# Optimization experiments

Hardware: AMD Instinct MI355X
Metric: run time of the kernel (lower is better)

The kernel has to match this reference:

```python
import jax, jax.numpy as jnp
import numpy as np

H = 256        # hidden_size
MAX_LEN = 200  # position table has MAX_LEN+1 rows
B = 4096       # number of sessions


def setup_inputs() -> dict:
    rng = np.random.RandomState(0)
    # ragged session lengths in [10, 100)
    seq_len = rng.randint(10, 100, size=B).astype(np.int64)
    T = int(seq_len.sum())
    # reverse positions: len-1, ..., 1, 0 per session (as the torch code uses)
    reverse_pos = np.concatenate([np.arange(l - 1, -1, -1) for l in seq_len]).astype(np.int64)

    key = jax.random.key(0)
    ks = jax.random.split(key, 8)
    def lin(k, fin, fout):
        # torch Linear init ~ U(-1/sqrt(fin), 1/sqrt(fin)); store as [fin, fout]
        lim = 1.0 / np.sqrt(fin)
        kw, kb = jax.random.split(k)
        W = jax.random.uniform(kw, (fin, fout), jnp.float32, -lim, lim)
        b = jax.random.uniform(kb, (fout,), jnp.float32, -lim, lim)
        return W, b

    hidden = jax.random.normal(ks[0], (T, H), jnp.float32)
    pos_table = jax.random.normal(ks[1], (MAX_LEN + 1, H), jnp.float32)
    W_pos, b_pos = lin(ks[2], 2 * H, H)   # W_pos_inter
    W1, b1 = lin(ks[3], H, H)             # W_1_inter
    W2, b2 = lin(ks[4], H, H)             # W_2_inter
    qw, qb = lin(ks[5], H, 1)             # q_inter

    return {
        "hidden": hidden,
        "pos_table": pos_table,
        "W_pos": W_pos, "b_pos": b_pos,
        "W1": W1, "b1": b1,
        "W2": W2, "b2": b2,
        "qw": qw, "qb": qb,
        "seq_len": jnp.asarray(seq_len),
        "reverse_pos": jnp.asarray(reverse_pos),
    }


def reference(hidden, pos_table, W_pos, b_pos, W1, b1, W2, b2, qw, qb, seq_len, reverse_pos):
    T = hidden.shape[0]
    nb = seq_len.shape[0]
    # segment id per token (sessions are contiguous)
    seg = jnp.repeat(jnp.arange(nb), seq_len, total_repeat_length=T)  # [T]
    # per-session mean, gathered back per token (v_mean_repeat_concat)
    sess_mean = jax.ops.segment_sum(hidden, seg, num_segments=nb)
    sess_mean = sess_mean / seq_len[:, None].astype(hidden.dtype)
    v_mean = sess_mean[seg]                                           # [T, H]
    # position-augmented hidden: tanh(W_pos_inter([hidden; pos_emb]))
    pos_emb = pos_table[reverse_pos]                                  # [T, H]
    pos_hidden = jnp.tanh(jnp.concatenate([hidden, pos_emb], -1) @ W_pos + b_pos)
    # alpha = q_inter(sigmoid(W_1_inter(v_mean) + W_2_inter(pos_hidden)))
    gate = jax.nn.sigmoid(v_mean @ W1 + b1 + pos_hidden @ W2 + b2)
    alpha = gate @ qw + qb                                            # [T, 1]
    # per-session weighted sum of hidden
    h_s = jax.ops.segment_sum(alpha * hidden, seg, num_segments=nb)   # [B, H]
    return h_s
```

## Files before the change

### kernel.cpp

```cpp
#include <hip/hip_runtime.h>
#include <hip/hip_bf16.h>
#include <stdint.h>

#define HD 256
#define BM 64
#define APAD 8
#define ASTRIDE (HD + APAD)

typedef __bf16 bf16x8 __attribute__((ext_vector_type(8)));
typedef float f32x4 __attribute__((ext_vector_type(4)));
typedef unsigned short ushort8v __attribute__((ext_vector_type(8)));
typedef unsigned short us4 __attribute__((ext_vector_type(4)));

__device__ __forceinline__ unsigned short f2bf(float f) {
    unsigned int x = __float_as_uint(f);
    unsigned int r = (x + 0x7FFFu + ((x >> 16) & 1u)) >> 16;
    return (unsigned short)r;
}

__global__ void scan_kernel(const int* __restrict__ seq_len, int* __restrict__ offsets, int B) {
    __shared__ int sums[256];
    int tid = threadIdx.x;
    int per = (B + 255) / 256;
    int b0 = tid * per;
    int local[32];
    int tot = 0;
    for (int i = 0; i < per && i < 32; ++i) {
        int b = b0 + i;
        int v = (b < B) ? seq_len[b] : 0;
        local[i] = tot;
        tot += v;
    }
    sums[tid] = tot;
    __syncthreads();
    for (int off = 1; off < 256; off <<= 1) {
        int v = (tid >= off) ? sums[tid - off] : 0;
        __syncthreads();
        sums[tid] += v;
        __syncthreads();
    }
    int start = sums[tid] - tot;
    for (int i = 0; i < per && i < 32; ++i) {
        int b = b0 + i;
        if (b < B) offsets[b] = start + local[i];
    }
    if (tid == 255) offsets[B] = sums[255];
}

__global__ void mean_kernel(const float* __restrict__ hidden, const int* __restrict__ offsets,
                            unsigned short* __restrict__ mean_bf, unsigned short* __restrict__ hb,
                            int* __restrict__ seg) {
    int b = blockIdx.x;
    int s = offsets[b], e = offsets[b + 1];
    int tid = threadIdx.x;
    for (int t = s + tid; t < e; t += 256) seg[t] = b;
    int g = tid >> 6, c = tid & 63;
    float4 acc = {0.f, 0.f, 0.f, 0.f};
    for (int t = s + g; t < e; t += 4) {
        const float4 v = *reinterpret_cast<const float4*>(hidden + (size_t)t * HD + c * 4);
        acc.x += v.x; acc.y += v.y; acc.z += v.z; acc.w += v.w;
        if (hb) {
            us4 pk;
            pk[0] = f2bf(v.x); pk[1] = f2bf(v.y); pk[2] = f2bf(v.z); pk[3] = f2bf(v.w);
            *reinterpret_cast<us4*>(hb + (size_t)t * HD + c * 4) = pk;
        }
    }
    __shared__ float4 part[4][64];
    part[g][c] = acc;
    __syncthreads();
    if (g == 0) {
        float4 a0 = part[0][c], a1 = part[1][c], a2 = part[2][c], a3 = part[3][c];
        float inv = 1.0f / (float)(e - s);
        us4 pk;
        pk[0] = f2bf((a0.x + a1.x + a2.x + a3.x) * inv);
        pk[1] = f2bf((a0.y + a1.y + a2.y + a3.y) * inv);
        pk[2] = f2bf((a0.z + a1.z + a2.z + a3.z) * inv);
        pk[3] = f2bf((a0.w + a1.w + a2.w + a3.w) * inv);
        *reinterpret_cast<us4*>(mean_bf + (size_t)b * HD + c * 4) = pk;
    }
}

__global__ void transpose_kernel(const float* __restrict__ Wp, const float* __restrict__ W1,
                                 const float* __restrict__ W2,
                                 unsigned short* __restrict__ WphT, unsigned short* __restrict__ WpbT,
                                 unsigned short* __restrict__ W1T, unsigned short* __restrict__ W2T) {
    __shared__ unsigned short tile[64][72];
    int bid = blockIdx.x;
    int tid = threadIdx.x;
    const float* src;
    unsigned short* dst;
    int k0, n0, kk;
    if (bid < 32) {
        int tk = bid >> 2, tn = bid & 3;
        src = Wp; k0 = tk * 64; n0 = tn * 64;
        if (k0 < 256) { dst = WphT; kk = k0; }
        else          { dst = WpbT; kk = k0 - 256; }
    } else if (bid < 48) {
        int b2 = bid - 32;
        src = W1; k0 = (b2 >> 2) * 64; n0 = (b2 & 3) * 64;
        dst = W1T; kk = k0;
    } else {
        int b2 = bid - 48;
        src = W2; k0 = (b2 >> 2) * 64; n0 = (b2 & 3) * 64;
        dst = W2T; kk = k0;
    }
    {
        int col = tid & 63;
        int rbase = tid >> 6;
        #pragma unroll
        for (int i = 0; i < 16; ++i) {
            int lrow = rbase + 4 * i;
            tile[lrow][col] = f2bf(src[(size_t)(k0 + lrow) * HD + n0 + col]);
        }
    }
    __syncthreads();
    {
        int nl = tid >> 2;
        int kc0 = (tid & 3) * 16;
        #pragma unroll
        for (int j = 0; j < 4; ++j) {
            int kc = kc0 + 4 * j;
            us4 v;
            v[0] = tile[kc + 0][nl];
            v[1] = tile[kc + 1][nl];
            v[2] = tile[kc + 2][nl];
            v[3] = tile[kc + 3][nl];
            *reinterpret_cast<us4*>(dst + (size_t)(n0 + nl) * HD + kk + kc) = v;
        }
    }
}

__global__ __launch_bounds__(256) void small_gemm_kernel(
    const unsigned short* __restrict__ mean_bf, int Mu, int nbu,
    const float* __restrict__ pos_table, int Mp,
    const unsigned short* __restrict__ W1T, const unsigned short* __restrict__ WpbT,
    const float* __restrict__ b1, const float* __restrict__ b2, const float* __restrict__ bp,
    float* __restrict__ u, float* __restrict__ P2) {
    __shared__ __align__(16) unsigned short As[16][ASTRIDE];
    int tid = threadIdx.x;
    bool isU = (int)blockIdx.x < nbu;
    int m0 = isU ? blockIdx.x * 16 : (blockIdx.x - nbu) * 16;
    int M  = isU ? Mu : Mp;
    const unsigned short* BT = isU ? W1T : WpbT;
    float* out = isU ? u : P2;

    {
        int row = tid >> 4;
        int colg = (tid & 15) * 16;
        int m = m0 + row;
        if (isU) {
            ushort8v v0 = {0,0,0,0,0,0,0,0}, v1 = {0,0,0,0,0,0,0,0};
            if (m < M) {
                v0 = *reinterpret_cast<const ushort8v*>(mean_bf + (size_t)m * HD + colg);
                v1 = *reinterpret_cast<const ushort8v*>(mean_bf + (size_t)m * HD + colg + 8);
            }
            *reinterpret_cast<ushort8v*>(&As[row][colg])     = v0;
            *reinterpret_cast<ushort8v*>(&As[row][colg + 8]) = v1;
        } else {
            float4 f[4] = {{0,0,0,0},{0,0,0,0},{0,0,0,0},{0,0,0,0}};
            if (m < M) {
                const float4* p = reinterpret_cast<const float4*>(pos_table + (size_t)m * HD + colg);
                f[0] = p[0]; f[1] = p[1]; f[2] = p[2]; f[3] = p[3];
            }
            ushort8v v0, v1;
            v0[0]=f2bf(f[0].x); v0[1]=f2bf(f[0].y); v0[2]=f2bf(f[0].z); v0[3]=f2bf(f[0].w);
            v0[4]=f2bf(f[1].x); v0[5]=f2bf(f[1].y); v0[6]=f2bf(f[1].z); v0[7]=f2bf(f[1].w);
            v1[0]=f2bf(f[2].x); v1[1]=f2bf(f[2].y); v1[2]=f2bf(f[2].z); v1[3]=f2bf(f[2].w);
            v1[4]=f2bf(f[3].x); v1[5]=f2bf(f[3].y); v1[6]=f2bf(f[3].z); v1[7]=f2bf(f[3].w);
            *reinterpret_cast<ushort8v*>(&As[row][colg])     = v0;
            *reinterpret_cast<ushort8v*>(&As[row][colg + 8]) = v1;
        }
    }
    __syncthreads();

    int wave = tid >> 6, lane = tid & 63, quad = lane >> 4, cc = lane & 15;
    int nb = wave * 64;
    f32x4 acc4[4];
    for (int i = 0; i < 4; ++i) acc4[i] = (f32x4){0.f, 0.f, 0.f, 0.f};

    bf16x8 wfp[4];
    for (int nf = 0; nf < 4; ++nf)
        wfp[nf] = *reinterpret_cast<const bf16x8*>(BT + (size_t)(nb + nf * 16 + cc) * HD + quad * 8);
    for (int kc8 = 0; kc8 < 8; ++kc8) {
        int kc = kc8 * 32;
        bf16x8 wfc[4];
        for (int nf = 0; nf < 4; ++nf) wfc[nf] = wfp[nf];
        if (kc8 < 7)
            for (int nf = 0; nf < 4; ++nf)
                wfp[nf] = *reinterpret_cast<const bf16x8*>(BT + (size_t)(nb + nf * 16 + cc) * HD + kc + 32 + quad * 8);
        bf16x8 af = *reinterpret_cast<const bf16x8*>(&As[cc][kc + quad * 8]);
        for (int nf = 0; nf < 4; ++nf)
            acc4[nf] = __builtin_amdgcn_mfma_f32_16x16x32_bf16(af, wfc[nf], acc4[nf], 0, 0, 0);
    }
    for (int nf = 0; nf < 4; ++nf)
        for (int r = 0; r < 4; ++r) {
            int row = m0 + quad * 4 + r;
            int col = nb + nf * 16 + cc;
            if (row < M) {
                float bias = isU ? (b1[col] + b2[col]) : bp[col];
                out[(size_t)row * HD + col] = acc4[nf][r] + bias;
            }
        }
}

__global__ __launch_bounds__(512, 4) void main_kernel(
    const float* __restrict__ hidden, const unsigned short* __restrict__ hb, int T,
    const unsigned short* __restrict__ WphT,
    const unsigned short* __restrict__ W2T,
    const float* __restrict__ P2,
    const float* __restrict__ u,
    const float* __restrict__ qw, const float* __restrict__ qb,
    const int* __restrict__ rp, const int* __restrict__ seg,
    float* __restrict__ alpha) {
    __shared__ __align__(16) unsigned short Ah[BM][ASTRIDE];
    __shared__ int rp_s[BM];
    __shared__ int seg_s[BM];
    __shared__ float alpha_s[BM];

    int tid = threadIdx.x;
    int t0 = blockIdx.x * BM;
    int wave = tid >> 6, lane = tid & 63, quad = lane >> 4, cc = lane & 15;
    int mb = wave * 32;

    bf16x8 afp[2];
    #pragma unroll
    for (int mf = 0; mf < 2; ++mf)
        afp[mf] = *reinterpret_cast<const bf16x8*>(WphT + (size_t)(mb + mf * 16 + cc) * HD + quad * 8);

    {
        int row = tid >> 3;
        int t = t0 + row;
        if (hb) {
            #pragma unroll
            for (int i = 0; i < 4; ++i) {
                int cg = (tid & 7) * 8 + 64 * i;
                ushort8v v = {0,0,0,0,0,0,0,0};
                if (t < T) v = *reinterpret_cast<const ushort8v*>(hb + (size_t)t * HD + cg);
                *reinterpret_cast<ushort8v*>(&Ah[row][cg]) = v;
            }
        } else {
            #pragma unroll
            for (int i = 0; i < 4; ++i) {
                int cg = (tid & 7) * 8 + 64 * i;
                float4 f0 = {0,0,0,0}, f1 = {0,0,0,0};
                if (t < T) {
                    const float4* p = reinterpret_cast<const float4*>(hidden + (size_t)t * HD + cg);
                    f0 = p[0]; f1 = p[1];
                }
                ushort8v pk;
                pk[0] = f2bf(f0.x); pk[1] = f2bf(f0.y); pk[2] = f2bf(f0.z); pk[3] = f2bf(f0.w);
                pk[4] = f2bf(f1.x); pk[5] = f2bf(f1.y); pk[6] = f2bf(f1.z); pk[7] = f2bf(f1.w);
                *reinterpret_cast<ushort8v*>(&Ah[row][cg]) = pk;
            }
        }
    }
    if (tid < BM) {
        int t = t0 + tid;
        rp_s[tid]  = (t < T) ? rp[t] : 0;
        seg_s[tid] = (t < T) ? seg[t] : 0;
        alpha_s[tid] = qb[0];
    }
    __syncthreads();

    f32x4 acc[2][4];
    #pragma unroll
    for (int i = 0; i < 2; ++i)
        #pragma unroll
        for (int j = 0; j < 4; ++j) acc[i][j] = (f32x4){0.f, 0.f, 0.f, 0.f};

    for (int kc8 = 0; kc8 < 8; ++kc8) {
        int kc = kc8 * 32;
        bf16x8 afc[2];
        #pragma unroll
        for (int mf = 0; mf < 2; ++mf) afc[mf] = afp[mf];
        if (kc8 < 7)
            #pragma unroll
            for (int mf = 0; mf < 2; ++mf)
                afp[mf] = *reinterpret_cast<const bf16x8*>(WphT + (size_t)(mb + mf * 16 + cc) * HD + kc + 32 + quad * 8);
        bf16x8 bfr[4];
        #pragma unroll
        for (int nf = 0; nf < 4; ++nf)
            bfr[nf] = *reinterpret_cast<const bf16x8*>(&Ah[nf * 16 + cc][kc + quad * 8]);
        #pragma unroll
        for (int mf = 0; mf < 2; ++mf)
            #pragma unroll
            for (int nf = 0; nf < 4; ++nf)
                acc[mf][nf] = __builtin_amdgcn_mfma_f32_16x16x32_bf16(afc[mf], bfr[nf], acc[mf][nf], 0, 0, 0);
    }
    __syncthreads();

    bf16x8 wfp[2];
    #pragma unroll
    for (int mf = 0; mf < 2; ++mf)
        wfp[mf] = *reinterpret_cast<const bf16x8*>(W2T + (size_t)(mb + mf * 16 + cc) * HD + quad * 8);

    #pragma unroll
    for (int nf = 0; nf < 4; ++nf) {
        int token = nf * 16 + cc;
        const float* p2row = P2 + (size_t)rp_s[token] * HD;
        #pragma unroll
        for (int mf = 0; mf < 2; ++mf) {
            int h0 = mb + mf * 16 + quad * 4;
            const float4 p2v = *reinterpret_cast<const float4*>(p2row + h0);
            us4 pk;
            {
                float v0 = acc[mf][nf][0] + p2v.x;
                float v1 = acc[mf][nf][1] + p2v.y;
                float v2 = acc[mf][nf][2] + p2v.z;
                float v3 = acc[mf][nf][3] + p2v.w;
                float e0 = __expf(2.f * v0), e1 = __expf(2.f * v1);
                float e2 = __expf(2.f * v2), e3 = __expf(2.f * v3);
                pk[0] = f2bf(1.f - 2.f / (e0 + 1.f));
                pk[1] = f2bf(1.f - 2.f / (e1 + 1.f));
                pk[2] = f2bf(1.f - 2.f / (e2 + 1.f));
                pk[3] = f2bf(1.f - 2.f / (e3 + 1.f));
            }
            *reinterpret_cast<us4*>(&Ah[token][h0]) = pk;
            acc[mf][nf] = (f32x4){0.f, 0.f, 0.f, 0.f};
        }
    }
    __syncthreads();

    for (int kc8 = 0; kc8 < 8; ++kc8) {
        int kc = kc8 * 32;
        bf16x8 wfc[2];
        #pragma unroll
        for (int mf = 0; mf < 2; ++mf) wfc[mf] = wfp[mf];
        if (kc8 < 7)
            #pragma unroll
            for (int mf = 0; mf < 2; ++mf)
                wfp[mf] = *reinterpret_cast<const bf16x8*>(W2T + (size_t)(mb + mf * 16 + cc) * HD + kc + 32 + quad * 8);
        #pragma unroll
        for (int nf = 0; nf < 4; ++nf) {
            bf16x8 af = *reinterpret_cast<const bf16x8*>(&Ah[nf * 16 + cc][kc + quad * 8]);
            #pragma unroll
            for (int mf = 0; mf < 2; ++mf)
                acc[mf][nf] = __builtin_amdgcn_mfma_f32_16x16x32_bf16(wfc[mf], af, acc[mf][nf], 0, 0, 0);
        }
    }

    float4 qv[2];
    #pragma unroll
    for (int mf = 0; mf < 2; ++mf)
        qv[mf] = *reinterpret_cast<const float4*>(qw + mb + mf * 16 + quad * 4);
    #pragma unroll
    for (int nf = 0; nf < 4; ++nf) {
        int token = nf * 16 + cc;
        const float* urow = u + (size_t)seg_s[token] * HD;
        float s = 0.f;
        #pragma unroll
        for (int mf = 0; mf < 2; ++mf) {
            int n0 = mb + mf * 16 + quad * 4;
            const float4 uv = *reinterpret_cast<const float4*>(urow + n0);
            #pragma unroll
            for (int r = 0; r < 4; ++r) {
                float g = acc[mf][nf][r] + ((const float*)&uv)[r];
                g = 1.0f / (1.0f + __expf(-g));
                s += g * ((const float*)&qv[mf])[r];
            }
        }
        s += __shfl_xor(s, 16);
        s += __shfl_xor(s, 32);
        if (quad == 0) atomicAdd(&alpha_s[token], s);
    }
    __syncthreads();
    if (tid < BM) {
        int t = t0 + tid;
        if (t < T) alpha[t] = alpha_s[tid];
    }
}

__global__ void hs_kernel(const float* __restrict__ hidden, const unsigned short* __restrict__ hb,
                          const float* __restrict__ alpha,
                          const int* __restrict__ offsets, float* __restrict__ out) {
    int b = blockIdx.x;
    int s = offsets[b], e = offsets[b + 1];
    int tid = threadIdx.x;
    __shared__ float al[256];
    for (int i = tid; i < e - s; i += 256) al[i] = alpha[s + i];
    __syncthreads();
    int g = tid >> 6, c = tid & 63;
    float4 acc = {0.f, 0.f, 0.f, 0.f};
    if (hb) {
        for (int t = s + g; t < e; t += 4) {
            float a = al[t - s];
            us4 v = *reinterpret_cast<const us4*>(hb + (size_t)t * HD + c * 4);
            acc.x += a * __uint_as_float(((unsigned)v[0]) << 16);
            acc.y += a * __uint_as_float(((unsigned)v[1]) << 16);
            acc.z += a * __uint_as_float(((unsigned)v[2]) << 16);
            acc.w += a * __uint_as_float(((unsigned)v[3]) << 16);
        }
    } else {
        for (int t = s + g; t < e; t += 4) {
            float a = al[t - s];
            const float4 v = *reinterpret_cast<const float4*>(hidden + (size_t)t * HD + c * 4);
            acc.x += a * v.x; acc.y += a * v.y; acc.z += a * v.z; acc.w += a * v.w;
        }
    }
    __shared__ float4 part[4][64];
    part[g][c] = acc;
    __syncthreads();
    if (g == 0) {
        float4 a0 = part[0][c], a1 = part[1][c], a2 = part[2][c], a3 = part[3][c];
        float4 m;
        m.x = a0.x + a1.x + a2.x + a3.x;
        m.y = a0.y + a1.y + a2.y + a3.y;
        m.z = a0.z + a1.z + a2.z + a3.z;
        m.w = a0.w + a1.w + a2.w + a3.w;
        *reinterpret_cast<float4*>(out + (size_t)b * HD + c * 4) = m;
    }
}

extern "C" void kernel_launch(void* const* d_in, const int* in_sizes, int n_in,
                              void* d_out, int out_size, void* d_ws, size_t ws_size,
                              hipStream_t stream) {
    (void)n_in; (void)out_size;
    const float* hidden    = (const float*)d_in[0];
    const float* pos_table = (const float*)d_in[1];
    const float* W_pos     = (const float*)d_in[2];
    const float* b_pos     = (const float*)d_in[3];
    const float* W1        = (const float*)d_in[4];
    const float* b1        = (const float*)d_in[5];
    const float* W2        = (const float*)d_in[6];
    const float* b2        = (const float*)d_in[7];
    const float* qw        = (const float*)d_in[8];
    const float* qb        = (const float*)d_in[9];
    const int* seq_len     = (const int*)d_in[10];
    const int* reverse_pos = (const int*)d_in[11];

    int T  = in_sizes[0] / HD;
    int B  = in_sizes[10];
    int NP = in_sizes[1] / HD;

    char* ws = (char*)d_ws;
    char* ws_end = ws + ws_size;
    auto carve = [&](size_t bytes) -> char* {
        char* p = ws;
        ws += (bytes + 255) & ~(size_t)255;
        return p;
    };
    int* offsets          = (int*)carve((size_t)(B + 1) * sizeof(int));
    int* seg              = (int*)carve((size_t)T * sizeof(int));
    unsigned short* meanb = (unsigned short*)carve((size_t)B * HD * 2);
    float* u              = (float*)carve((size_t)B * HD * sizeof(float));
    float* P2             = (float*)carve((size_t)NP * HD * sizeof(float));
    unsigned short* WphT  = (unsigned short*)carve((size_t)HD * HD * 2);
    unsigned short* WpbT  = (unsigned short*)carve((size_t)HD * HD * 2);
    unsigned short* W1T   = (unsigned short*)carve((size_t)HD * HD * 2);
    unsigned short* W2T   = (unsigned short*)carve((size_t)HD * HD * 2);
    float* alpha          = (float*)carve((size_t)T * sizeof(float));
    unsigned short* hb    = nullptr;
    if ((size_t)(ws_end - ws) >= (size_t)T * HD * 2 + 256)
        hb = (unsigned short*)carve((size_t)T * HD * 2);

    int nbu = (B + 15) / 16;
    int nbp = (NP + 15) / 16;

    scan_kernel<<<1, 256, 0, stream>>>(seq_len, offsets, B);
    transpose_kernel<<<64, 256, 0, stream>>>(W_pos, W1, W2, WphT, WpbT, W1T, W2T);
    mean_kernel<<<B, 256, 0, stream>>>(hidden, offsets, meanb, hb, seg);
    small_gemm_kernel<<<nbu + nbp, 256, 0, stream>>>(meanb, B, nbu, pos_table, NP,
                                                     W1T, WpbT, b1, b2, b_pos, u, P2);
    main_kernel<<<(T + BM - 1) / BM, 512, 0, stream>>>(hidden, hb, T, WphT, W2T, P2, u, qw, qb,
                                                       reverse_pos, seg, alpha);
    hs_kernel<<<B, 256, 0, stream>>>(hidden, hb, alpha, offsets, (float*)d_out);
}
```

Baseline: 561.1 us.

## Merge prep kernels, use one wave per session, prefetch gathered rows

Merges the scan and weight-transpose kernels into one launch. The mean and weighted-sum kernels now give each session a single wavefront that walks its tokens serially, which removes the shared-memory partial reduction and block barriers. In the main kernel, the gathered P2 and u rows are loaded early so their latency overlaps the MFMA loops. The trade-off is less memory-level parallelism per session in the reduction kernels and higher register pressure in the main kernel.

```diff
diff --git a/kernel.cpp b/kernel.cpp
--- a/kernel.cpp
+++ b/kernel.cpp
@@ -18,116 +18,117 @@
     return (unsigned short)r;
 }
 
-__global__ void scan_kernel(const int* __restrict__ seq_len, int* __restrict__ offsets, int B) {
-    __shared__ int sums[256];
+__global__ void prep_kernel(const int* __restrict__ seq_len, int* __restrict__ offsets, int B,
+                            const float* __restrict__ Wp, const float* __restrict__ W1,
+                            const float* __restrict__ W2,
+                            unsigned short* __restrict__ WphT, unsigned short* __restrict__ WpbT,
+                            unsigned short* __restrict__ W1T, unsigned short* __restrict__ W2T) {
     int tid = threadIdx.x;
-    int per = (B + 255) / 256;
-    int b0 = tid * per;
-    int local[32];
-    int tot = 0;
-    for (int i = 0; i < per && i < 32; ++i) {
-        int b = b0 + i;
-        int v = (b < B) ? seq_len[b] : 0;
-        local[i] = tot;
-        tot += v;
-    }
-    sums[tid] = tot;
-    __syncthreads();
-    for (int off = 1; off < 256; off <<= 1) {
-        int v = (tid >= off) ? sums[tid - off] : 0;
+    if (blockIdx.x == 0) {
+        __shared__ int sums[256];
+        int per = (B + 255) / 256;
+        int b0 = tid * per;
+        int local[32];
+        int tot = 0;
+        for (int i = 0; i < per && i < 32; ++i) {
+            int b = b0 + i;
+            int v = (b < B) ? seq_len[b] : 0;
+            local[i] = tot;
+            tot += v;
+        }
+        sums[tid] = tot;
         __syncthreads();
-        sums[tid] += v;
+        for (int off = 1; off < 256; off <<= 1) {
+            int v = (tid >= off) ? sums[tid - off] : 0;
+            __syncthreads();
+            sums[tid] += v;
+            __syncthreads();
+        }
+        int start = sums[tid] - tot;
+        for (int i = 0; i < per && i < 32; ++i) {
+            int b = b0 + i;
+            if (b < B) offsets[b] = start + local[i];
+        }
+        if (tid == 255) offsets[B] = sums[255];
+    } else {
+        __shared__ unsigned short tile[64][72];
+        int bid = blockIdx.x - 1;
+        const float* src;
+        unsigned short* dst;
+        int k0, n0, kk;
+        if (bid < 32) {
+            int tk = bid >> 2, tn = bid & 3;
+            src = Wp; k0 = tk * 64; n0 = tn * 64;
+            if (k0 < 256) { dst = WphT; kk = k0; }
+            else          { dst = WpbT; kk = k0 - 256; }
+        } else if (bid < 48) {
+            int b2 = bid - 32;
+            src = W1; k0 = (b2 >> 2) * 64; n0 = (b2 & 3) * 64;
+            dst = W1T; kk = k0;
+        } else {
+            int b2 = bid - 48;
+            src = W2; k0 = (b2 >> 2) * 64; n0 = (b2 & 3) * 64;
+            dst = W2T; kk = k0;
+        }
+        {
+            int col = tid & 63;
+            int rbase = tid >> 6;
+            #pragma unroll
+            for (int i = 0; i < 16; ++i) {
+                int lrow = rbase + 4 * i;
+                tile[lrow][col] = f2bf(src[(size_t)(k0 + lrow) * HD + n0 + col]);
+            }
+        }
         __syncthreads();
-    }
-    int start = sums[tid] - tot;
-    for (int i = 0; i < per && i < 32; ++i) {
-        int b = b0 + i;
-        if (b < B) offsets[b] = start + local[i];
-    }
-    if (tid == 255) offsets[B] = sums[255];
-}
-
-__global__ void mean_kernel(const float* __restrict__ hidden, const int* __restrict__ offsets,
-                            unsigned short* __restrict__ mean_bf, unsigned short* __restrict__ hb,
-                            int* __restrict__ seg) {
-    int b = blockIdx.x;
+        {
+            int nl = tid >> 2;
+            int kc0 = (tid & 3) * 16;
+            #pragma unroll
+            for (int j = 0; j < 4; ++j) {
+                int kc = kc0 + 4 * j;
+                us4 v;
+                v[0] = tile[kc + 0][nl];
+                v[1] = tile[kc + 1][nl];
+                v[2] = tile[kc + 2][nl];
+                v[3] = tile[kc + 3][nl];
+                *reinterpret_cast<us4*>(dst + (size_t)(n0 + nl) * HD + kk + kc) = v;
+            }
+        }
+    }
+}
+
+__global__ __launch_bounds__(256) void mean_kernel(
+    const float* __restrict__ hidden, const int* __restrict__ offsets,
+    unsigned short* __restrict__ mean_bf, unsigned short* __restrict__ hb,
+    int* __restrict__ seg, int B) {
+    int wave = threadIdx.x >> 6, lane = threadIdx.x & 63;
+    int b = blockIdx.x * 4 + wave;
+    if (b >= B) return;
     int s = offsets[b], e = offsets[b + 1];
-    int tid = threadIdx.x;
-    for (int t = s + tid; t < e; t += 256) seg[t] = b;
-    int g = tid >> 6, c = tid & 63;
+    for (int t = s + lane; t < e; t += 64) seg[t] = b;
+    int c4 = lane * 4;
     float4 acc = {0.f, 0.f, 0.f, 0.f};
-    for (int t = s + g; t < e; t += 4) {
-        const float4 v = *reinterpret_cast<const float4*>(hidden + (size_t)t * HD + c * 4);
-        acc.x += v.x; acc.y += v.y; acc.z += v.z; acc.w += v.w;
-        if (hb) {
+    if (hb) {
+        for (int t = s; t < e; ++t) {
+            const float4 v = *reinterpret_cast<const float4*>(hidden + (size_t)t * HD + c4);
+            acc.x += v.x; acc.y += v.y; acc.z += v.z; acc.w += v.w;
             us4 pk;
             pk[0] = f2bf(v.x); pk[1] = f2bf(v.y); pk[2] = f2bf(v.z); pk[3] = f2bf(v.w);
-            *reinterpret_cast<us4*>(hb + (size_t)t * HD + c * 4) = pk;
-        }
-    }
-    __shared__ float4 part[4][64];
-    part[g][c] = acc;
-    __syncthreads();
-    if (g == 0) {
-        float4 a0 = part[0][c], a1 = part[1][c], a2 = part[2][c], a3 = part[3][c];
-        float inv = 1.0f / (float)(e - s);
-        us4 pk;
-        pk[0] = f2bf((a0.x + a1.x + a2.x + a3.x) * inv);
-        pk[1] = f2bf((a0.y + a1.y + a2.y + a3.y) * inv);
-        pk[2] = f2bf((a0.z + a1.z + a2.z + a3.z) * inv);
-        pk[3] = f2bf((a0.w + a1.w + a2.w + a3.w) * inv);
-        *reinterpret_cast<us4*>(mean_bf + (size_t)b * HD + c * 4) = pk;
-    }
-}
-
-__global__ void transpose_kernel(const float* __restrict__ Wp, const float* __restrict__ W1,
-                                 const float* __restrict__ W2,
-                                 unsigned short* __restrict__ WphT, unsigned short* __restrict__ WpbT,
-                                 unsigned short* __restrict__ W1T, unsigned short* __restrict__ W2T) {
-    __shared__ unsigned short tile[64][72];
-    int bid = blockIdx.x;
-    int tid = threadIdx.x;
-    const float* src;
-    unsigned short* dst;
-    int k0, n0, kk;
-    if (bid < 32) {
-        int tk = bid >> 2, tn = bid & 3;
-        src = Wp; k0 = tk * 64; n0 = tn * 64;
-        if (k0 < 256) { dst = WphT; kk = k0; }
-        else          { dst = WpbT; kk = k0 - 256; }
-    } else if (bid < 48) {
-        int b2 = bid - 32;
-        src = W1; k0 = (b2 >> 2) * 64; n0 = (b2 & 3) * 64;
-        dst = W1T; kk = k0;
+            *reinterpret_cast<us4*>(hb + (size_t)t * HD + c4) = pk;
+        }
     } else {
-        int b2 = bid - 48;
-        src = W2; k0 = (b2 >> 2) * 64; n0 = (b2 & 3) * 64;
-        dst = W2T; kk = k0;
-    }
-    {
-        int col = tid & 63;
-        int rbase = tid >> 6;
-        #pragma unroll
-        for (int i = 0; i < 16; ++i) {
-            int lrow = rbase + 4 * i;
-            tile[lrow][col] = f2bf(src[(size_t)(k0 + lrow) * HD + n0 + col]);
-        }
-    }
-    __syncthreads();
-    {
-        int nl = tid >> 2;
-        int kc0 = (tid & 3) * 16;
-        #pragma unroll
-        for (int j = 0; j < 4; ++j) {
-            int kc = kc0 + 4 * j;
-            us4 v;
-            v[0] = tile[kc + 0][nl];
-            v[1] = tile[kc + 1][nl];
-            v[2] = tile[kc + 2][nl];
-            v[3] = tile[kc + 3][nl];
-            *reinterpret_cast<us4*>(dst + (size_t)(n0 + nl) * HD + kk + kc) = v;
-        }
-    }
+        for (int t = s; t < e; ++t) {
+            const float4 v = *reinterpret_cast<const float4*>(hidden + (size_t)t * HD + c4);
+            acc.x += v.x; acc.y += v.y; acc.z += v.z; acc.w += v.w;
+        }
+    }
+    float inv = 1.0f / (float)(e - s);
+    us4 pk;
+    pk[0] = f2bf(acc.x * inv);
+    pk[1] = f2bf(acc.y * inv);
+    pk[2] = f2bf(acc.z * inv);
+    pk[3] = f2bf(acc.w * inv);
+    *reinterpret_cast<us4*>(mean_bf + (size_t)b * HD + c4) = pk;
 }
 
 __global__ __launch_bounds__(256) void small_gemm_kernel(
@@ -287,6 +288,15 @@
             for (int nf = 0; nf < 4; ++nf)
                 acc[mf][nf] = __builtin_amdgcn_mfma_f32_16x16x32_bf16(afc[mf], bfr[nf], acc[mf][nf], 0, 0, 0);
     }
+
+    f32x4 p2v[4][2];
+    #pragma unroll
+    for (int nf = 0; nf < 4; ++nf) {
+        const float* p2row = P2 + (size_t)rp_s[nf * 16 + cc] * HD;
+        #pragma unroll
+        for (int mf = 0; mf < 2; ++mf)
+            p2v[nf][mf] = *reinterpret_cast<const f32x4*>(p2row + mb + mf * 16 + quad * 4);
+    }
     __syncthreads();
 
     bf16x8 wfp[2];
@@ -297,17 +307,15 @@
     #pragma unroll
     for (int nf = 0; nf < 4; ++nf) {
         int token = nf * 16 + cc;
-        const float* p2row = P2 + (size_t)rp_s[token] * HD;
         #pragma unroll
         for (int mf = 0; mf < 2; ++mf) {
             int h0 = mb + mf * 16 + quad * 4;
-            const float4 p2v = *reinterpret_cast<const float4*>(p2row + h0);
             us4 pk;
             {
-                float v0 = acc[mf][nf][0] + p2v.x;
-                float v1 = acc[mf][nf][1] + p2v.y;
-                float v2 = acc[mf][nf][2] + p2v.z;
-                float v3 = acc[mf][nf][3] + p2v.w;
+                float v0 = acc[mf][nf][0] + p2v[nf][mf][0];
+                float v1 = acc[mf][nf][1] + p2v[nf][mf][1];
+                float v2 = acc[mf][nf][2] + p2v[nf][mf][2];
+                float v3 = acc[mf][nf][3] + p2v[nf][mf][3];
                 float e0 = __expf(2.f * v0), e1 = __expf(2.f * v1);
                 float e2 = __expf(2.f * v2), e3 = __expf(2.f * v3);
                 pk[0] = f2bf(1.f - 2.f / (e0 + 1.f));
@@ -321,6 +329,19 @@
     }
     __syncthreads();
 
+    f32x4 uv[4][2];
+    #pragma unroll
+    for (int nf = 0; nf < 4; ++nf) {
+        const float* urow = u + (size_t)seg_s[nf * 16 + cc] * HD;
+        #pragma unroll
+        for (int mf = 0; mf < 2; ++mf)
+            uv[nf][mf] = *reinterpret_cast<const f32x4*>(urow + mb + mf * 16 + quad * 4);
+    }
+    f32x4 qv[2];
+    #pragma unroll
+    for (int mf = 0; mf < 2; ++mf)
+        qv[mf] = *reinterpret_cast<const f32x4*>(qw + mb + mf * 16 + quad * 4);
+
     for (int kc8 = 0; kc8 < 8; ++kc8) {
         int kc = kc8 * 32;
         bf16x8 wfc[2];
@@ -339,24 +360,17 @@
         }
     }
 
-    float4 qv[2];
-    #pragma unroll
-    for (int mf = 0; mf < 2; ++mf)
-        qv[mf] = *reinterpret_cast<const float4*>(qw + mb + mf * 16 + quad * 4);
     #pragma unroll
     for (int nf = 0; nf < 4; ++nf) {
         int token = nf * 16 + cc;
-        const float* urow = u + (size_t)seg_s[token] * HD;
         float s = 0.f;
         #pragma unroll
         for (int mf = 0; mf < 2; ++mf) {
-            int n0 = mb + mf * 16 + quad * 4;
-            const float4 uv = *reinterpret_cast<const float4*>(urow + n0);
             #pragma unroll
             for (int r = 0; r < 4; ++r) {
-                float g = acc[mf][nf][r] + ((const float*)&uv)[r];
+                float g = acc[mf][nf][r] + uv[nf][mf][r];
                 g = 1.0f / (1.0f + __expf(-g));
-                s += g * ((const float*)&qv[mf])[r];
+                s += g * qv[mf][r];
             }
         }
         s += __shfl_xor(s, 16);
@@ -370,45 +384,33 @@
     }
 }
 
-__global__ void hs_kernel(const float* __restrict__ hidden, const unsigned short* __restrict__ hb,
-                          const float* __restrict__ alpha,
-                          const int* __restrict__ offsets, float* __restrict__ out) {
-    int b = blockIdx.x;
+__global__ __launch_bounds__(256) void hs_kernel(
+    const float* __restrict__ hidden, const unsigned short* __restrict__ hb,
+    const float* __restrict__ alpha,
+    const int* __restrict__ offsets, float* __restrict__ out, int B) {
+    int wave = threadIdx.x >> 6, lane = threadIdx.x & 63;
+    int b = blockIdx.x * 4 + wave;
+    if (b >= B) return;
     int s = offsets[b], e = offsets[b + 1];
-    int tid = threadIdx.x;
-    __shared__ float al[256];
-    for (int i = tid; i < e - s; i += 256) al[i] = alpha[s + i];
-    __syncthreads();
-    int g = tid >> 6, c = tid & 63;
+    int c4 = lane * 4;
     float4 acc = {0.f, 0.f, 0.f, 0.f};
     if (hb) {
-        for (int t = s + g; t < e; t += 4) {
-            float a = al[t - s];
-            us4 v = *reinterpret_cast<const us4*>(hb + (size_t)t * HD + c * 4);
+        for (int t = s; t < e; ++t) {
+            float a = alpha[t];
+            us4 v = *reinterpret_cast<const us4*>(hb + (size_t)t * HD + c4);
             acc.x += a * __uint_as_float(((unsigned)v[0]) << 16);
             acc.y += a * __uint_as_float(((unsigned)v[1]) << 16);
             acc.z += a * __uint_as_float(((unsigned)v[2]) << 16);
             acc.w += a * __uint_as_float(((unsigned)v[3]) << 16);
         }
     } else {
-        for (int t = s + g; t < e; t += 4) {
-            float a = al[t - s];
-            const float4 v = *reinterpret_cast<const float4*>(hidden + (size_t)t * HD + c * 4);
+        for (int t = s; t < e; ++t) {
+            float a = alpha[t];
+            const float4 v = *reinterpret_cast<const float4*>(hidden + (size_t)t * HD + c4);
             acc.x += a * v.x; acc.y += a * v.y; acc.z += a * v.z; acc.w += a * v.w;
         }
     }
-    __shared__ float4 part[4][64];
-    part[g][c] = acc;
-    __syncthreads();
-    if (g == 0) {
-        float4 a0 = part[0][c], a1 = part[1][c], a2 = part[2][c], a3 = part[3][c];
-        float4 m;
-        m.x = a0.x + a1.x + a2.x + a3.x;
-        m.y = a0.y + a1.y + a2.y + a3.y;
-        m.z = a0.z + a1.z + a2.z + a3.z;
-        m.w = a0.w + a1.w + a2.w + a3.w;
-        *reinterpret_cast<float4*>(out + (size_t)b * HD + c * 4) = m;
-    }
+    *reinterpret_cast<float4*>(out + (size_t)b * HD + c4) = acc;
 }
 
 extern "C" void kernel_launch(void* const* d_in, const int* in_sizes, int n_in,
@@ -455,13 +457,14 @@
 
     int nbu = (B + 15) / 16;
     int nbp = (NP + 15) / 16;
-
-    scan_kernel<<<1, 256, 0, stream>>>(seq_len, offsets, B);
-    transpose_kernel<<<64, 256, 0, stream>>>(W_pos, W1, W2, WphT, WpbT, W1T, W2T);
-    mean_kernel<<<B, 256, 0, stream>>>(hidden, offsets, meanb, hb, seg);
+    int nsb = (B + 3) / 4;
+
+    prep_kernel<<<65, 256, 0, stream>>>(seq_len, offsets, B, W_pos, W1, W2,
+                                        WphT, WpbT, W1T, W2T);
+    mean_kernel<<<nsb, 256, 0, stream>>>(hidden, offsets, meanb, hb, seg, B);
     small_gemm_kernel<<<nbu + nbp, 256, 0, stream>>>(meanb, B, nbu, pos_table, NP,
                                                      W1T, WpbT, b1, b2, b_pos, u, P2);
     main_kernel<<<(T + BM - 1) / BM, 512, 0, stream>>>(hidden, hb, T, WphT, W2T, P2, u, qw, qb,
                                                        reverse_pos, seg, alpha);
-    hs_kernel<<<B, 256, 0, stream>>>(hidden, hb, alpha, offsets, (float*)d_out);
-}
+    hs_kernel<<<nsb, 256, 0, stream>>>(hidden, hb, alpha, offsets, (float*)d_out, B);
+}
```

New measurement: 578.3 us. +3.1%, slower.
